# Performance work log

Hardware: AMD Instinct MI355X
Metric: run time of the kernel (lower is better)

Reference implementation:

```python
import jax, jax.numpy as jnp
import numpy as np

B, T, IN, H, L = 64, 512, 512, 512, 2


def setup_inputs() -> dict:
    key = jax.random.key(0)
    ks = jax.random.split(key, 7)
    s_ih = 1.0 / np.sqrt(H)
    x = jax.random.normal(ks[0], (B, T, IN), dtype=jnp.float32)
    encoder_h = jax.random.normal(ks[1], (L, B, H), dtype=jnp.float32)
    # stacked GRUCell params per layer (input_size == hidden_size so stackable)
    W_ih = jax.random.uniform(ks[2], (L, 3 * H, IN), jnp.float32, -s_ih, s_ih)
    W_hh = jax.random.uniform(ks[3], (L, 3 * H, H), jnp.float32, -s_ih, s_ih)
    b_ih = jax.random.uniform(ks[4], (L, 3 * H), jnp.float32, -s_ih, s_ih)
    b_hh = jax.random.uniform(ks[5], (L, 3 * H), jnp.float32, -s_ih, s_ih)
    return {"x": x, "encoder_h": encoder_h, "W_ih": W_ih, "W_hh": W_hh,
            "b_ih": b_ih, "b_hh": b_hh}


def _gru_cell(x, h, W_ih, W_hh, b_ih, b_hh):
    # torch.nn.GRUCell math
    gi = x @ W_ih.T + b_ih            # [B, 3H]
    gh = h @ W_hh.T + b_hh            # [B, 3H]
    i_r, i_z, i_n = jnp.split(gi, 3, axis=-1)
    h_r, h_z, h_n = jnp.split(gh, 3, axis=-1)
    r = jax.nn.sigmoid(i_r + h_r)
    z = jax.nn.sigmoid(i_z + h_z)
    n = jnp.tanh(i_n + r * h_n)
    return (1.0 - z) * n + z * h


def reference(x, encoder_h, W_ih, W_hh, b_ih, b_hh):
    num_layers = W_ih.shape[0]

    def step(h_carry, x_t):
        hs = []
        inp = x_t
        for j in range(num_layers):  # small static layer loop
            h_new = _gru_cell(inp, h_carry[j], W_ih[j], W_hh[j], b_ih[j], b_hh[j])
            hs.append(h_new)
            inp = h_new
        return tuple(hs), inp

    h0 = tuple(encoder_h[j] for j in range(num_layers))
    xs = jnp.swapaxes(x, 0, 1)                 # [T, B, IN]
    h_final, outs = jax.lax.scan(step, h0, xs)  # outs: [T, B, H]
    out = jnp.swapaxes(outs, 0, 1)             # [B, T, H]
    h = jnp.stack(h_final, axis=0)             # [L, B, H]
    return out, h
```

## Files before the change

kernel.cpp:

```cpp
#include <hip/hip_runtime.h>


#define NBLK 256
#define NTHR 512
#define Bsz  64
#define Tlen 512
#define Kd   512
#define Hd   512
#define KC   64
#define LP   67

__device__ __forceinline__ float sigf(float v){ return 1.0f/(1.0f+__expf(-v)); }
__device__ __forceinline__ float tanhx(float v){
  float e=__expf(-2.0f*fabsf(v)); float t=(1.0f-e)/(1.0f+e); return v<0.0f?-t:t;
}
__device__ __forceinline__ unsigned umin2(unsigned a, unsigned b){ return a<b?a:b; }

__device__ __forceinline__ void st_coh(float* p, float v){
  asm volatile("global_store_dword %0, %1, off sc0 sc1" :: "v"(p), "v"(v) : "memory");
}
__device__ __forceinline__ void st_coh_u(unsigned* p, unsigned v){
  asm volatile("global_store_dword %0, %1, off sc0 sc1" :: "v"(p), "v"(v) : "memory");
}
__device__ __forceinline__ void wait_vm0(){ asm volatile("s_waitcnt vmcnt(0)" ::: "memory"); }

__device__ __forceinline__ void grid_barrier(unsigned* slots, unsigned target, int tid){
  wait_vm0();
  __syncthreads();
  if(tid == 0) st_coh_u(slots + blockIdx.x, target);
  if(tid < 64){
    const unsigned* p0 = slots + tid;
    for(;;){
      unsigned a,b,c,d;
      asm volatile(
        "global_load_dword %0, %4, off sc0 sc1\n\t"
        "global_load_dword %1, %5, off sc0 sc1\n\t"
        "global_load_dword %2, %6, off sc0 sc1\n\t"
        "global_load_dword %3, %7, off sc0 sc1\n\t"
        "s_waitcnt vmcnt(0)"
        : "=v"(a),"=v"(b),"=v"(c),"=v"(d)
        : "v"(p0), "v"(p0+64), "v"(p0+128), "v"(p0+192)
        : "memory");
      unsigned m = umin2(umin2(a,b), umin2(c,d));
      #pragma unroll
      for(int off=32; off; off>>=1)
        m = umin2(m, (unsigned)__shfl_xor((int)m, off, 64));
      if(m >= target) break;
      __builtin_amdgcn_s_sleep(1);
    }
  }
  __syncthreads();
  __builtin_amdgcn_fence(__ATOMIC_ACQUIRE, "agent");
}

__device__ __forceinline__ void stageA(float* sbuf, const float* __restrict__ x,
                                       int t, int ch, int tid){
  #pragma unroll
  for(int it=0; it<2; ++it){
    int q  = it*NTHR + tid;
    int b  = q >> 4;
    int k4 = (q & 15) << 2;
    const float4 v = *(const float4*)(x + ((size_t)b*Tlen + t)*Kd + ch*KC + k4);
    sbuf[(k4+0)*LP + b] = v.x;
    sbuf[(k4+1)*LP + b] = v.y;
    sbuf[(k4+2)*LP + b] = v.z;
    sbuf[(k4+3)*LP + b] = v.w;
  }
}

__device__ __forceinline__ void gru_fma(const float* __restrict__ wlds, int kg,
                                        const float* xv, const float* hv,
                                        float* pr, float* pz, float* pni, float* pnh)
{
  float4 w[24];
  #pragma unroll
  for(int s = 0; s < 24; ++s)
    w[s] = *(const float4*)(wlds + s*Kd + kg);
  #pragma unroll
  for(int u = 0; u < 4; ++u){
    #pragma unroll
    for(int c = 0; c < 4; ++c){
      pr[c]  = fmaf(xv[u], (&w[     c].x)[u], pr[c]);
      pz[c]  = fmaf(xv[u], (&w[ 4 + c].x)[u], pz[c]);
      pni[c] = fmaf(xv[u], (&w[ 8 + c].x)[u], pni[c]);
      pr[c]  = fmaf(hv[u], (&w[12 + c].x)[u], pr[c]);
      pz[c]  = fmaf(hv[u], (&w[16 + c].x)[u], pz[c]);
      pnh[c] = fmaf(hv[u], (&w[20 + c].x)[u], pnh[c]);
    }
  }
}

extern "C" __global__ void __launch_bounds__(NTHR, 2)
gru_persist(const float* __restrict__ x,
            const float* __restrict__ eh,
            const float* __restrict__ Wih,
            const float* __restrict__ Whh,
            const float* __restrict__ bih,
            const float* __restrict__ bhh,
            float* __restrict__ out,
            float* __restrict__ ws)
{
  __shared__ float smem[2*KC*LP];
  __shared__ float wlds[24*Kd];

  unsigned* slots = (unsigned*)ws;
  float* h0T = ws + 256;
  float* h1T = h0T + 2*Kd*Bsz;
  float* htail = out + (size_t)Bsz*Tlen*Hd;

  const int tid  = threadIdx.x;
  const int lane = tid & 63;
  const int wv   = __builtin_amdgcn_readfirstlane(tid >> 6);
  const int cell = blockIdx.x >> 7;
  const int cb   = blockIdx.x & 127;
  const int col0 = cb * 4;
  unsigned bar = 1;

  {
    const float* WiC = Wih + (size_t)cell*3*Hd*Kd;
    const float* WhC = Whh + (size_t)cell*3*Hd*Kd;
    #pragma unroll 1
    for(int i = tid; i < 24*(Kd/4); i += NTHR){
      const int s   = i >> 7;
      const int k4  = (i & 127) << 2;
      const int mat = (s >= 12);
      const int r   = s - 12*mat;
      const int g   = r >> 2, c = r & 3;
      const float* src = (mat ? WhC : WiC) + ((size_t)(g*Hd + col0 + c))*Kd + k4;
      *(float4*)(wlds + (size_t)s*Kd + k4) = *(const float4*)src;
    }
  }

  {
    int i = blockIdx.x*NTHR + tid;
    if(i < 2*Kd*Bsz){
      int l = i >> 15, k = (i >> 6) & 511, b = i & 63;
      float v = eh[(size_t)(l*Bsz + b)*Hd + k];
      st_coh((l ? h1T : h0T) + Kd*Bsz + k*Bsz + b, v);
    }
  }
  grid_barrier(slots, bar, tid); bar++;

  const int ec = wv & 3;
  const int ecol = col0 + ec;
  const float bi0 = bih[cell*1536 + 0*Hd + ecol] + bhh[cell*1536 + 0*Hd + ecol];
  const float bi1 = bih[cell*1536 + 1*Hd + ecol] + bhh[cell*1536 + 1*Hd + ecol];
  const float bi2 = bih[cell*1536 + 2*Hd + ecol];
  const float bh2 = bhh[cell*1536 + 2*Hd + ecol];

  for(int t = 0; t <= Tlen; ++t){
    const bool active = (cell == 0) ? (t < Tlen) : (t >= 1);
    if(active){
      const int s = (cell == 0) ? t : (t - 1);
      float* hbase = (cell == 0) ? h0T : h1T;
      const float* hprev = hbase + ((s+1)&1)*Kd*Bsz;
      float*       hout  = hbase + (s&1)*Kd*Bsz;
      const float* inT   = h0T + (s&1)*Kd*Bsz;

      float pr[4]={0,0,0,0}, pz[4]={0,0,0,0}, pni[4]={0,0,0,0}, pnh[4]={0,0,0,0};

      if(cell == 0){
        stageA(smem, x, t, 0, tid);
        __syncthreads();
        for(int ch = 0; ch < 8; ++ch){
          const float* cur = smem + (ch&1)*(KC*LP);
          if(ch < 7) stageA(smem + ((ch+1)&1)*(KC*LP), x, t, ch+1, tid);
          #pragma unroll
          for(int jj = 0; jj < 8; jj += 4){
            const int kl = (wv<<3) + jj;
            const int kg = (ch<<6) + kl;
            float xv[4], hv[4];
            #pragma unroll
            for(int u = 0; u < 4; ++u){
              xv[u] = cur[(kl+u)*LP + lane];
              hv[u] = hprev[(kg+u)*Bsz + lane];
            }
            gru_fma(wlds, kg, xv, hv, pr, pz, pni, pnh);
          }
          __syncthreads();
        }
      } else {
        const int kg0 = (wv<<6);
        float xv[4], hv[4], xn[4], hn[4];
        #pragma unroll
        for(int u = 0; u < 4; ++u){
          xv[u] = inT[(kg0+u)*Bsz + lane];
          hv[u] = hprev[(kg0+u)*Bsz + lane];
        }
        #pragma unroll 1
        for(int j4 = 0; j4 < 60; j4 += 4){
          const int kg = kg0 + j4;
          #pragma unroll
          for(int u = 0; u < 4; ++u){
            xn[u] = inT[(kg+4+u)*Bsz + lane];
            hn[u] = hprev[(kg+4+u)*Bsz + lane];
          }
          gru_fma(wlds, kg, xv, hv, pr, pz, pni, pnh);
          #pragma unroll
          for(int u = 0; u < 4; ++u){ xv[u] = xn[u]; hv[u] = hn[u]; }
        }
        gru_fma(wlds, kg0 + 60, xv, hv, pr, pz, pni, pnh);
        __syncthreads();
      }

      float* red = smem;
      #pragma unroll
      for(int c = 0; c < 4; ++c){
        red[(((c<<2)+0)*8 + wv)*64 + lane] = pr[c];
        red[(((c<<2)+1)*8 + wv)*64 + lane] = pz[c];
        red[(((c<<2)+2)*8 + wv)*64 + lane] = pni[c];
        red[(((c<<2)+3)*8 + wv)*64 + lane] = pnh[c];
      }
      __syncthreads();
      if(wv < 4){
        const int c = wv;
        float spr=0.f, spz=0.f, spni=0.f, spnh=0.f;
        #pragma unroll
        for(int w = 0; w < 8; ++w){
          spr  += red[(((c<<2)+0)*8 + w)*64 + lane];
          spz  += red[(((c<<2)+1)*8 + w)*64 + lane];
          spni += red[(((c<<2)+2)*8 + w)*64 + lane];
          spnh += red[(((c<<2)+3)*8 + w)*64 + lane];
        }
        const int col = col0 + c;
        const float hkeep = hprev[col*Bsz + lane];
        const float r = sigf(spr + bi0);
        const float z = sigf(spz + bi1);
        const float n = tanhx(spni + bi2 + r*(spnh + bh2));
        const float hnew = (1.0f - z)*n + z*hkeep;
        st_coh(hout + col*Bsz + lane, hnew);
        if(cell == 1)
          out[((size_t)lane*Tlen + s)*Hd + col] = hnew;
      }
    }
    grid_barrier(slots, bar, tid); bar++;
  }

  {
    int i = blockIdx.x*NTHR + tid;
    if(i < 2*Kd*Bsz){
      int l = i >> 15, b = (i >> 9) & 63, c = i & 511;
      const float* src = (l ? h1T : h0T) + Kd*Bsz;
      htail[i] = src[c*Bsz + b];
    }
  }
}

extern "C" void kernel_launch(void* const* d_in, const int* in_sizes, int n_in,
                              void* d_out, int out_size, void* d_ws, size_t ws_size,
                              hipStream_t stream) {
  (void)in_sizes; (void)n_in; (void)out_size; (void)ws_size;
  const float* x   = (const float*)d_in[0];
  const float* eh  = (const float*)d_in[1];
  const float* Wih = (const float*)d_in[2];
  const float* Whh = (const float*)d_in[3];
  const float* bih = (const float*)d_in[4];
  const float* bhh = (const float*)d_in[5];
  float* out = (float*)d_out;
  float* ws  = (float*)d_ws;

  hipMemsetAsync(d_ws, 0, 1024, stream);

  void* args[] = {(void*)&x, (void*)&eh, (void*)&Wih, (void*)&Whh,
                  (void*)&bih, (void*)&bhh, (void*)&out, (void*)&ws};
  hipLaunchCooperativeKernel((const void*)gru_persist, dim3(NBLK), dim3(NTHR),
                             args, 0, stream);
}
```

Measured before the change: 19.72 ms.

## Use striped atomic counters for grid barrier and prefetch x during wait

```diff
diff --git a/kernel.cpp b/kernel.cpp
--- a/kernel.cpp
+++ b/kernel.cpp
@@ -14,44 +14,11 @@
 __device__ __forceinline__ float tanhx(float v){
   float e=__expf(-2.0f*fabsf(v)); float t=(1.0f-e)/(1.0f+e); return v<0.0f?-t:t;
 }
-__device__ __forceinline__ unsigned umin2(unsigned a, unsigned b){ return a<b?a:b; }
 
 __device__ __forceinline__ void st_coh(float* p, float v){
   asm volatile("global_store_dword %0, %1, off sc0 sc1" :: "v"(p), "v"(v) : "memory");
 }
-__device__ __forceinline__ void st_coh_u(unsigned* p, unsigned v){
-  asm volatile("global_store_dword %0, %1, off sc0 sc1" :: "v"(p), "v"(v) : "memory");
-}
 __device__ __forceinline__ void wait_vm0(){ asm volatile("s_waitcnt vmcnt(0)" ::: "memory"); }
-
-__device__ __forceinline__ void grid_barrier(unsigned* slots, unsigned target, int tid){
-  wait_vm0();
-  __syncthreads();
-  if(tid == 0) st_coh_u(slots + blockIdx.x, target);
-  if(tid < 64){
-    const unsigned* p0 = slots + tid;
-    for(;;){
-      unsigned a,b,c,d;
-      asm volatile(
-        "global_load_dword %0, %4, off sc0 sc1\n\t"
-        "global_load_dword %1, %5, off sc0 sc1\n\t"
-        "global_load_dword %2, %6, off sc0 sc1\n\t"
-        "global_load_dword %3, %7, off sc0 sc1\n\t"
-        "s_waitcnt vmcnt(0)"
-        : "=v"(a),"=v"(b),"=v"(c),"=v"(d)
-        : "v"(p0), "v"(p0+64), "v"(p0+128), "v"(p0+192)
-        : "memory");
-      unsigned m = umin2(umin2(a,b), umin2(c,d));
-      #pragma unroll
-      for(int off=32; off; off>>=1)
-        m = umin2(m, (unsigned)__shfl_xor((int)m, off, 64));
-      if(m >= target) break;
-      __builtin_amdgcn_s_sleep(1);
-    }
-  }
-  __syncthreads();
-  __builtin_amdgcn_fence(__ATOMIC_ACQUIRE, "agent");
-}
 
 __device__ __forceinline__ void stageA(float* sbuf, const float* __restrict__ x,
                                        int t, int ch, int tid){
@@ -66,6 +33,38 @@
     sbuf[(k4+2)*LP + b] = v.z;
     sbuf[(k4+3)*LP + b] = v.w;
   }
+}
+
+__device__ __forceinline__ void grid_barrier(unsigned* cnt8, unsigned target, int tid,
+                                             bool ps, float* sbuf,
+                                             const float* __restrict__ x, int tn){
+  wait_vm0();
+  __syncthreads();
+  if(tid == 0) atomicAdd(cnt8 + ((blockIdx.x & 7) << 4), 1u);
+  if(ps) stageA(sbuf, x, tn, 0, tid);
+  if(tid == 0){
+    const unsigned tgt = target << 8;
+    for(;;){
+      unsigned c0,c1,c2,c3,c4,c5,c6,c7;
+      asm volatile(
+        "global_load_dword %0, %8, off sc0 sc1\n\t"
+        "global_load_dword %1, %8, off offset:64 sc0 sc1\n\t"
+        "global_load_dword %2, %8, off offset:128 sc0 sc1\n\t"
+        "global_load_dword %3, %8, off offset:192 sc0 sc1\n\t"
+        "global_load_dword %4, %8, off offset:256 sc0 sc1\n\t"
+        "global_load_dword %5, %8, off offset:320 sc0 sc1\n\t"
+        "global_load_dword %6, %8, off offset:384 sc0 sc1\n\t"
+        "global_load_dword %7, %8, off offset:448 sc0 sc1\n\t"
+        "s_waitcnt vmcnt(0)"
+        : "=&v"(c0),"=&v"(c1),"=&v"(c2),"=&v"(c3),
+          "=&v"(c4),"=&v"(c5),"=&v"(c6),"=&v"(c7)
+        : "v"(cnt8) : "memory");
+      if(((c0+c1)+(c2+c3))+((c4+c5)+(c6+c7)) >= tgt) break;
+      __builtin_amdgcn_s_sleep(1);
+    }
+  }
+  __syncthreads();
+  __builtin_amdgcn_fence(__ATOMIC_ACQUIRE, "agent");
 }
 
 __device__ __forceinline__ void gru_fma(const float* __restrict__ wlds, int kg,
@@ -103,7 +102,7 @@
   __shared__ float smem[2*KC*LP];
   __shared__ float wlds[24*Kd];
 
-  unsigned* slots = (unsigned*)ws;
+  unsigned* cnt8 = (unsigned*)ws;
   float* h0T = ws + 256;
   float* h1T = h0T + 2*Kd*Bsz;
   float* htail = out + (size_t)Bsz*Tlen*Hd;
@@ -139,7 +138,7 @@
       st_coh((l ? h1T : h0T) + Kd*Bsz + k*Bsz + b, v);
     }
   }
-  grid_barrier(slots, bar, tid); bar++;
+  grid_barrier(cnt8, bar, tid, cell==0, smem, x, 0); bar++;
 
   const int ec = wv & 3;
   const int ecol = col0 + ec;
@@ -160,8 +159,7 @@
       float pr[4]={0,0,0,0}, pz[4]={0,0,0,0}, pni[4]={0,0,0,0}, pnh[4]={0,0,0,0};
 
       if(cell == 0){
-        stageA(smem, x, t, 0, tid);
-        __syncthreads();
+        #pragma unroll
         for(int ch = 0; ch < 8; ++ch){
           const float* cur = smem + (ch&1)*(KC*LP);
           if(ch < 7) stageA(smem + ((ch+1)&1)*(KC*LP), x, t, ch+1, tid);
@@ -181,25 +179,17 @@
         }
       } else {
         const int kg0 = (wv<<6);
-        float xv[4], hv[4], xn[4], hn[4];
-        #pragma unroll
-        for(int u = 0; u < 4; ++u){
-          xv[u] = inT[(kg0+u)*Bsz + lane];
-          hv[u] = hprev[(kg0+u)*Bsz + lane];
-        }
         #pragma unroll 1
-        for(int j4 = 0; j4 < 60; j4 += 4){
+        for(int j4 = 0; j4 < 64; j4 += 4){
           const int kg = kg0 + j4;
+          float xv[4], hv[4];
           #pragma unroll
           for(int u = 0; u < 4; ++u){
-            xn[u] = inT[(kg+4+u)*Bsz + lane];
-            hn[u] = hprev[(kg+4+u)*Bsz + lane];
+            xv[u] = inT[(kg+u)*Bsz + lane];
+            hv[u] = hprev[(kg+u)*Bsz + lane];
           }
           gru_fma(wlds, kg, xv, hv, pr, pz, pni, pnh);
-          #pragma unroll
-          for(int u = 0; u < 4; ++u){ xv[u] = xn[u]; hv[u] = hn[u]; }
         }
-        gru_fma(wlds, kg0 + 60, xv, hv, pr, pz, pni, pnh);
         __syncthreads();
       }
 
@@ -233,7 +223,7 @@
           out[((size_t)lane*Tlen + s)*Hd + col] = hnew;
       }
     }
-    grid_barrier(slots, bar, tid); bar++;
+    grid_barrier(cnt8, bar, tid, cell==0 && (t+1) < Tlen, smem, x, t+1); bar++;
   }
 
   {
```

New measurement: 41.75 ms. +111.8%, slower.
